# Performance work log

Hardware: AMD Instinct MI355X
Metric: run time of the kernel (lower is better)

## Reference

```python
import jax, jax.numpy as jnp
import numpy as np

B, S, H, E = 4, 4096, 4096, 64
TOP_K = 2


def setup_inputs() -> dict:
    key = jax.random.key(0)
    k1, k2 = jax.random.split(key)
    x = jax.random.normal(k1, (B, S, H), dtype=jnp.float32)
    # nn.Linear weight: [num_experts, hidden_size]
    gate_w = jax.random.normal(k2, (E, H), dtype=jnp.float32) * (1.0 / np.sqrt(H))
    return {"x": x, "gate_w": gate_w}


def reference(x, gate_w):
    # gate linear: [B,S,H] @ [H,E] -> [B,S,E]
    router_logits = jnp.einsum("bsh,eh->bse", x, gate_w)
    router_weights = jax.nn.softmax(router_logits, axis=-1)
    topk_weights, topk_indices = jax.lax.top_k(router_weights, TOP_K)  # [B,S,2]
    topk_weights = topk_weights / jnp.sum(topk_weights, axis=-1, keepdims=True)
    return topk_weights, topk_indices
```

## Files before the change

kernel.cpp:

```cpp
#include <hip/hip_runtime.h>
#include <math.h>


typedef _Float16 half8 __attribute__((ext_vector_type(8)));
typedef float floatx4 __attribute__((ext_vector_type(4)));

constexpr int Hdim = 4096;
constexpr int Edim = 64;
constexpr int NTOK = 16384;
constexpr int BK   = 128;
constexpr int NKT  = Hdim / BK;
constexpr float SCL  = 2048.0f;
constexpr float ISCL = 1.0f / 2048.0f;

__device__ alignas(16) _Float16 g_whf[(size_t)Edim * Hdim];
__device__ alignas(16) _Float16 g_wlf[(size_t)Edim * Hdim];

#define GLD_LDS16(gp, lp)                                              \
    __builtin_amdgcn_global_load_lds(                                  \
        (const __attribute__((address_space(1))) void*)(gp),           \
        (__attribute__((address_space(3))) void*)(lp), 16, 0, 0)

__global__ __launch_bounds__(256)
void wconv_kernel(const float* __restrict__ gw)
{
    const int n    = blockIdx.x * 256 + threadIdx.x;
    const int lane = n & 63;
    const int frag = n >> 6;
    const int nt   = frag & 3;
    const int kc   = frag >> 2;
    const int e    = nt * 16 + (lane & 15);
    const int k0   = kc * 32 + (lane >> 4) * 8;

    const float* src = gw + (size_t)e * Hdim + k0;
    const float4 v0 = *(const float4*)src;
    const float4 v1 = *(const float4*)(src + 4);
    const float* p0 = (const float*)&v0;
    const float* p1 = (const float*)&v1;
    half8 h, l;
    #pragma unroll
    for (int c = 0; c < 4; ++c) {
        _Float16 hh = (_Float16)p0[c];
        h[c] = hh;
        l[c] = (_Float16)((p0[c] - (float)hh) * SCL);
        hh = (_Float16)p1[c];
        h[c + 4] = hh;
        l[c + 4] = (_Float16)((p1[c] - (float)hh) * SCL);
    }
    *(half8*)(g_whf + (size_t)n * 8) = h;
    *(half8*)(g_wlf + (size_t)n * 8) = l;
}

__global__ __launch_bounds__(256, 4)
void router_kernel(const float* __restrict__ x,
                   float* __restrict__ out)
{
    __shared__ alignas(16) float  sx[3][16 * BK];
    __shared__ alignas(16) float4 sc[4][16];

    const int tid  = threadIdx.x;
    const int w    = tid >> 6;
    const int lane = tid & 63;
    const int ln15 = lane & 15;
    const int quad = lane >> 4;
    const int sw   = ln15 & 7;
    const int t0   = blockIdx.x * 16;

    const int r0 = w * 4 + (lane >> 5);
    const int r1 = r0 + 2;
    const int g0 = (lane & 31) ^ (r0 & 7);
    const int g1 = (lane & 31) ^ (r1 & 7);
    const float* px0 = x + (size_t)(t0 + r0) * Hdim + g0 * 4;
    const float* px1 = x + (size_t)(t0 + r1) * Hdim + g1 * 4;

    const _Float16* whw = g_whf + (size_t)w * 512 + lane * 8;
    const _Float16* wlw = g_wlf + (size_t)w * 512 + lane * 8;

    floatx4 accm = (floatx4)0.0f, accc = (floatx4)0.0f, accl = (floatx4)0.0f;

    auto cvt8 = [&](const float4& a, const float4& b, half8& h, half8& l) {
        const float* pa = (const float*)&a;
        const float* pb = (const float*)&b;
        #pragma unroll
        for (int c = 0; c < 4; ++c) {
            _Float16 hh = (_Float16)pa[c];
            h[c] = hh;
            l[c] = (_Float16)((pa[c] - (float)hh) * SCL);
            hh = (_Float16)pb[c];
            h[c + 4] = hh;
            l[c + 4] = (_Float16)((pb[c] - (float)hh) * SCL);
        }
    };

    half8 bhA[4], blA[4], bhB[4], blB[4];

    #pragma unroll
    for (int c = 0; c < 4; ++c) {
        bhA[c] = *(const half8*)(whw + (size_t)c * 2048);
        blA[c] = *(const half8*)(wlw + (size_t)c * 2048);
    }
    GLD_LDS16(px0,      &sx[0][w * 512]);
    GLD_LDS16(px1,      &sx[0][w * 512 + 256]);
    GLD_LDS16(px0 + BK, &sx[1][w * 512]);
    GLD_LDS16(px1 + BK, &sx[1][w * 512 + 256]);

    auto step = [&](int kt, half8 (&bch)[4], half8 (&bcl)[4],
                            half8 (&bnh)[4], half8 (&bnl)[4]) {
        const int ktn = (kt + 1) & (NKT - 1);
        #pragma unroll
        for (int c = 0; c < 4; ++c) {
            bnh[c] = *(const half8*)(whw + (size_t)(ktn * 4 + c) * 2048);
            bnl[c] = *(const half8*)(wlw + (size_t)(ktn * 4 + c) * 2048);
        }
        __builtin_amdgcn_sched_barrier(0);

        const int ts = (kt + 2) & (NKT - 1);
        const int tb = (kt + 2) % 3;
        GLD_LDS16(px0 + (size_t)ts * BK, &sx[tb][w * 512]);
        GLD_LDS16(px1 + (size_t)ts * BK, &sx[tb][w * 512 + 256]);

        asm volatile("s_waitcnt vmcnt(12)" ::: "memory");
        asm volatile("s_barrier" ::: "memory");

        const int cur = kt % 3;
        #pragma unroll
        for (int c = 0; c < 4; ++c) {
            const int s0 = (c * 8 + quad * 2) ^ sw;
            const float4 f0 = *(const float4*)&sx[cur][ln15 * BK + s0 * 4];
            const float4 f1 = *(const float4*)&sx[cur][ln15 * BK + (s0 ^ 1) * 4];
            half8 ah, al;
            cvt8(f0, f1, ah, al);
            accm = __builtin_amdgcn_mfma_f32_16x16x32_f16(ah, bch[c], accm, 0, 0, 0);
            accc = __builtin_amdgcn_mfma_f32_16x16x32_f16(ah, bcl[c], accc, 0, 0, 0);
            accc = __builtin_amdgcn_mfma_f32_16x16x32_f16(al, bch[c], accc, 0, 0, 0);
            accl = __builtin_amdgcn_mfma_f32_16x16x32_f16(al, bcl[c], accl, 0, 0, 0);
        }
        asm volatile("s_barrier" ::: "memory");
    };

    for (int kt = 0; kt < NKT; kt += 2) {
        step(kt,     bhA, blA, bhB, blB);
        step(kt + 1, bhB, blB, bhA, blA);
    }
    __syncthreads();

    const floatx4 vv = accm + accc * ISCL + accl * (ISCL * ISCL);

    #pragma unroll
    for (int i = 0; i < 4; ++i) {
        float m1 = vv[i], m2 = -INFINITY;
        int i1 = w * 16 + ln15, i2 = 0;
        #pragma unroll
        for (int mk = 1; mk <= 8; mk <<= 1) {
            const float om1 = __shfl_xor(m1, mk);
            const int   oi1 = __shfl_xor(i1, mk);
            const float om2 = __shfl_xor(m2, mk);
            const int   oi2 = __shfl_xor(i2, mk);
            const bool aw = (m1 > om1) || (m1 == om1 && i1 < oi1);
            const float w1v = aw ? m1 : om1;  const int w1i = aw ? i1 : oi1;
            const float ca  = aw ? m2 : om2;  const int cai = aw ? i2 : oi2;
            const float cb  = aw ? om1 : m1;  const int cbi = aw ? oi1 : i1;
            const bool sw2 = (ca > cb) || (ca == cb && cai < cbi);
            m1 = w1v; i1 = w1i;
            m2 = sw2 ? ca : cb;
            i2 = sw2 ? cai : cbi;
        }
        if (ln15 == 0)
            sc[w][quad * 4 + i] = float4{m1, m2, (float)i1, (float)i2};
    }
    __syncthreads();

    if (tid < 16) {
        float4 c = sc[0][tid];
        float m1 = c.x, m2 = c.y, i1 = c.z, i2 = c.w;
        #pragma unroll
        for (int q = 1; q < 4; ++q) {
            c = sc[q][tid];
            const float om1 = c.x, om2 = c.y, oi1 = c.z, oi2 = c.w;
            const bool aw = (m1 > om1) || (m1 == om1 && i1 < oi1);
            const float w1v = aw ? m1 : om1;  const float w1i = aw ? i1 : oi1;
            const float ca  = aw ? m2 : om2;  const float cai = aw ? i2 : oi2;
            const float cb  = aw ? om1 : m1;  const float cbi = aw ? oi1 : i1;
            const bool sw2 = (ca > cb) || (ca == cb && cai < cbi);
            m1 = w1v; i1 = w1i;
            m2 = sw2 ? ca : cb;
            i2 = sw2 ? cai : cbi;
        }
        const float r   = expf(m2 - m1);
        const float inv = 1.0f / (1.0f + r);
        const int t = t0 + tid;
        float* ow = out + 2 * (size_t)t;
        ow[0] = inv;
        ow[1] = r * inv;
        float* oi = out + 2 * (size_t)NTOK + 2 * (size_t)t;
        oi[0] = i1;
        oi[1] = i2;
    }
}

extern "C" void kernel_launch(void* const* d_in, const int* in_sizes, int n_in,
                              void* d_out, int out_size, void* d_ws, size_t ws_size,
                              hipStream_t stream) {
    const float* x  = (const float*)d_in[0];
    const float* gw = (const float*)d_in[1];
    float* out = (float*)d_out;
    (void)d_ws; (void)ws_size;

    hipLaunchKernelGGL(wconv_kernel, dim3(128), dim3(256), 0, stream, gw);
    hipLaunchKernelGGL(router_kernel, dim3(NTOK / 16), dim3(256), 0, stream,
                       x, out);
}
```

Measured before the change: 376.2 us.

## Convert x tile to fp16 hi/lo once in LDS and double token tile

Before, each of the four waves converted the same 16 token rows from fp32 to the fp16 hi/lo split for its own 16 experts, so the conversion ran four times. Now each tile is converted once cooperatively into shared fp16 buffers, and the block covers 32 tokens with two M-tiles per wave. This halves the weight-fragment loads per token and removes the redundant conversion work. In exchange it adds LDS traffic, an extra conversion stage in the pipeline, more registers and LDS per block, and occupancy drops from 4 to 3 blocks.

```diff
diff --git a/kernel.cpp b/kernel.cpp
--- a/kernel.cpp
+++ b/kernel.cpp
@@ -8,7 +8,8 @@
 constexpr int Hdim = 4096;
 constexpr int Edim = 64;
 constexpr int NTOK = 16384;
-constexpr int BK   = 128;
+constexpr int BM   = 32;
+constexpr int BK   = 64;
 constexpr int NKT  = Hdim / BK;
 constexpr float SCL  = 2048.0f;
 constexpr float ISCL = 1.0f / 2048.0f;
@@ -51,32 +52,46 @@
     *(half8*)(g_wlf + (size_t)n * 8) = l;
 }
 
-__global__ __launch_bounds__(256, 4)
+__global__ __launch_bounds__(256, 3)
 void router_kernel(const float* __restrict__ x,
                    float* __restrict__ out)
 {
-    __shared__ alignas(16) float  sx[3][16 * BK];
-    __shared__ alignas(16) float4 sc[4][16];
+    __shared__ alignas(16) float    sraw[3][BM * BK];
+    __shared__ alignas(16) _Float16 sxh[2][BM * BK];
+    __shared__ alignas(16) _Float16 sxl[2][BM * BK];
+    __shared__ alignas(16) float4   sc[4][BM];
 
     const int tid  = threadIdx.x;
     const int w    = tid >> 6;
     const int lane = tid & 63;
     const int ln15 = lane & 15;
     const int quad = lane >> 4;
-    const int sw   = ln15 & 7;
-    const int t0   = blockIdx.x * 16;
-
-    const int r0 = w * 4 + (lane >> 5);
-    const int r1 = r0 + 2;
-    const int g0 = (lane & 31) ^ (r0 & 7);
-    const int g1 = (lane & 31) ^ (r1 & 7);
-    const float* px0 = x + (size_t)(t0 + r0) * Hdim + g0 * 4;
-    const float* px1 = x + (size_t)(t0 + r1) * Hdim + g1 * 4;
+    const int t0   = blockIdx.x * BM;
+
+    const int r0  = 8 * w + (lane >> 4);
+    const int r1  = r0 + 4;
+    const int gg0 = (lane & 15) ^ (r0 & 7);
+    const int gg1 = (lane & 15) ^ (r1 & 7);
+    const float* px0 = x + (size_t)(t0 + r0) * Hdim + gg0 * 4;
+    const float* px1 = x + (size_t)(t0 + r1) * Hdim + gg1 * 4;
+
+    const int cr  = 8 * w + ((tid >> 3) & 7);
+    const int cc  = tid & 7;
+    const int crs = cr & 7;
+    const int rdA = cr * BK + (((2 * cc)     ^ crs) << 2);
+    const int rdB = cr * BK + (((2 * cc + 1) ^ crs) << 2);
+    const int wrS = cr * BK + ((cc ^ crs) << 3);
 
     const _Float16* whw = g_whf + (size_t)w * 512 + lane * 8;
     const _Float16* wlw = g_wlf + (size_t)w * 512 + lane * 8;
 
-    floatx4 accm = (floatx4)0.0f, accc = (floatx4)0.0f, accl = (floatx4)0.0f;
+    floatx4 accm[2], accc[2], accl[2];
+    #pragma unroll
+    for (int mt = 0; mt < 2; ++mt) {
+        accm[mt] = (floatx4)0.0f;
+        accc[mt] = (floatx4)0.0f;
+        accl[mt] = (floatx4)0.0f;
+    }
 
     auto cvt8 = [&](const float4& a, const float4& b, half8& h, half8& l) {
         const float* pa = (const float*)&a;
@@ -92,50 +107,67 @@
         }
     };
 
-    half8 bhA[4], blA[4], bhB[4], blB[4];
-
-    #pragma unroll
-    for (int c = 0; c < 4; ++c) {
+    auto convert = [&](int rb, int sb) {
+        const float4 f0 = *(const float4*)&sraw[rb][rdA];
+        const float4 f1 = *(const float4*)&sraw[rb][rdB];
+        half8 h, l;
+        cvt8(f0, f1, h, l);
+        *(half8*)&sxh[sb][wrS] = h;
+        *(half8*)&sxl[sb][wrS] = l;
+    };
+
+    half8 bhA[2], blA[2], bhB[2], blB[2];
+
+    GLD_LDS16(px0 + 0 * BK, &sraw[0][(8 * w) * BK]);
+    GLD_LDS16(px1 + 0 * BK, &sraw[0][(8 * w + 4) * BK]);
+    GLD_LDS16(px0 + 1 * BK, &sraw[1][(8 * w) * BK]);
+    GLD_LDS16(px1 + 1 * BK, &sraw[1][(8 * w + 4) * BK]);
+    #pragma unroll
+    for (int c = 0; c < 2; ++c) {
         bhA[c] = *(const half8*)(whw + (size_t)c * 2048);
         blA[c] = *(const half8*)(wlw + (size_t)c * 2048);
     }
-    GLD_LDS16(px0,      &sx[0][w * 512]);
-    GLD_LDS16(px1,      &sx[0][w * 512 + 256]);
-    GLD_LDS16(px0 + BK, &sx[1][w * 512]);
-    GLD_LDS16(px1 + BK, &sx[1][w * 512 + 256]);
-
-    auto step = [&](int kt, half8 (&bch)[4], half8 (&bcl)[4],
-                            half8 (&bnh)[4], half8 (&bnl)[4]) {
+    GLD_LDS16(px0 + 2 * BK, &sraw[2][(8 * w) * BK]);
+    GLD_LDS16(px1 + 2 * BK, &sraw[2][(8 * w + 4) * BK]);
+
+    asm volatile("s_waitcnt vmcnt(8)" ::: "memory");
+    convert(0, 0);
+
+    auto step = [&](int kt, half8 (&bch)[2], half8 (&bcl)[2],
+                            half8 (&bnh)[2], half8 (&bnl)[2]) {
         const int ktn = (kt + 1) & (NKT - 1);
         #pragma unroll
-        for (int c = 0; c < 4; ++c) {
-            bnh[c] = *(const half8*)(whw + (size_t)(ktn * 4 + c) * 2048);
-            bnl[c] = *(const half8*)(wlw + (size_t)(ktn * 4 + c) * 2048);
-        }
+        for (int c = 0; c < 2; ++c) {
+            bnh[c] = *(const half8*)(whw + (size_t)(2 * ktn + c) * 2048);
+            bnl[c] = *(const half8*)(wlw + (size_t)(2 * ktn + c) * 2048);
+        }
+        const int ts = (kt + 3) & (NKT - 1);
+        const int tb = (kt + 3) % 3;
+        GLD_LDS16(px0 + (size_t)ts * BK, &sraw[tb][(8 * w) * BK]);
+        GLD_LDS16(px1 + (size_t)ts * BK, &sraw[tb][(8 * w + 4) * BK]);
+
+        asm volatile("s_waitcnt vmcnt(8)" ::: "memory");
+        asm volatile("s_waitcnt lgkmcnt(0)" ::: "memory");
         __builtin_amdgcn_sched_barrier(0);
-
-        const int ts = (kt + 2) & (NKT - 1);
-        const int tb = (kt + 2) % 3;
-        GLD_LDS16(px0 + (size_t)ts * BK, &sx[tb][w * 512]);
-        GLD_LDS16(px1 + (size_t)ts * BK, &sx[tb][w * 512 + 256]);
-
-        asm volatile("s_waitcnt vmcnt(12)" ::: "memory");
         asm volatile("s_barrier" ::: "memory");
 
-        const int cur = kt % 3;
-        #pragma unroll
-        for (int c = 0; c < 4; ++c) {
-            const int s0 = (c * 8 + quad * 2) ^ sw;
-            const float4 f0 = *(const float4*)&sx[cur][ln15 * BK + s0 * 4];
-            const float4 f1 = *(const float4*)&sx[cur][ln15 * BK + (s0 ^ 1) * 4];
-            half8 ah, al;
-            cvt8(f0, f1, ah, al);
-            accm = __builtin_amdgcn_mfma_f32_16x16x32_f16(ah, bch[c], accm, 0, 0, 0);
-            accc = __builtin_amdgcn_mfma_f32_16x16x32_f16(ah, bcl[c], accc, 0, 0, 0);
-            accc = __builtin_amdgcn_mfma_f32_16x16x32_f16(al, bch[c], accc, 0, 0, 0);
-            accl = __builtin_amdgcn_mfma_f32_16x16x32_f16(al, bcl[c], accl, 0, 0, 0);
-        }
-        asm volatile("s_barrier" ::: "memory");
+        convert((kt + 1) % 3, (kt + 1) & 1);
+
+        const int cb = kt & 1;
+        #pragma unroll
+        for (int c = 0; c < 2; ++c) {
+            #pragma unroll
+            for (int mt = 0; mt < 2; ++mt) {
+                const int row = mt * 16 + ln15;
+                const int sA  = row * BK + (((c * 4 + quad) ^ (row & 7)) << 3);
+                const half8 ah = *(const half8*)&sxh[cb][sA];
+                const half8 al = *(const half8*)&sxl[cb][sA];
+                accm[mt] = __builtin_amdgcn_mfma_f32_16x16x32_f16(ah, bch[c], accm[mt], 0, 0, 0);
+                accc[mt] = __builtin_amdgcn_mfma_f32_16x16x32_f16(ah, bcl[c], accc[mt], 0, 0, 0);
+                accc[mt] = __builtin_amdgcn_mfma_f32_16x16x32_f16(al, bch[c], accc[mt], 0, 0, 0);
+                accl[mt] = __builtin_amdgcn_mfma_f32_16x16x32_f16(al, bcl[c], accl[mt], 0, 0, 0);
+            }
+        }
     };
 
     for (int kt = 0; kt < NKT; kt += 2) {
@@ -144,33 +176,35 @@
     }
     __syncthreads();
 
-    const floatx4 vv = accm + accc * ISCL + accl * (ISCL * ISCL);
-
-    #pragma unroll
-    for (int i = 0; i < 4; ++i) {
-        float m1 = vv[i], m2 = -INFINITY;
-        int i1 = w * 16 + ln15, i2 = 0;
-        #pragma unroll
-        for (int mk = 1; mk <= 8; mk <<= 1) {
-            const float om1 = __shfl_xor(m1, mk);
-            const int   oi1 = __shfl_xor(i1, mk);
-            const float om2 = __shfl_xor(m2, mk);
-            const int   oi2 = __shfl_xor(i2, mk);
-            const bool aw = (m1 > om1) || (m1 == om1 && i1 < oi1);
-            const float w1v = aw ? m1 : om1;  const int w1i = aw ? i1 : oi1;
-            const float ca  = aw ? m2 : om2;  const int cai = aw ? i2 : oi2;
-            const float cb  = aw ? om1 : m1;  const int cbi = aw ? oi1 : i1;
-            const bool sw2 = (ca > cb) || (ca == cb && cai < cbi);
-            m1 = w1v; i1 = w1i;
-            m2 = sw2 ? ca : cb;
-            i2 = sw2 ? cai : cbi;
-        }
-        if (ln15 == 0)
-            sc[w][quad * 4 + i] = float4{m1, m2, (float)i1, (float)i2};
+    #pragma unroll
+    for (int mt = 0; mt < 2; ++mt) {
+        const floatx4 vv = accm[mt] + accc[mt] * ISCL + accl[mt] * (ISCL * ISCL);
+        #pragma unroll
+        for (int i = 0; i < 4; ++i) {
+            float m1 = vv[i], m2 = -INFINITY;
+            int i1 = w * 16 + ln15, i2 = 0;
+            #pragma unroll
+            for (int mk = 1; mk <= 8; mk <<= 1) {
+                const float om1 = __shfl_xor(m1, mk);
+                const int   oi1 = __shfl_xor(i1, mk);
+                const float om2 = __shfl_xor(m2, mk);
+                const int   oi2 = __shfl_xor(i2, mk);
+                const bool aw = (m1 > om1) || (m1 == om1 && i1 < oi1);
+                const float w1v = aw ? m1 : om1;  const int w1i = aw ? i1 : oi1;
+                const float ca  = aw ? m2 : om2;  const int cai = aw ? i2 : oi2;
+                const float cb  = aw ? om1 : m1;  const int cbi = aw ? oi1 : i1;
+                const bool sw2 = (ca > cb) || (ca == cb && cai < cbi);
+                m1 = w1v; i1 = w1i;
+                m2 = sw2 ? ca : cb;
+                i2 = sw2 ? cai : cbi;
+            }
+            if (ln15 == 0)
+                sc[w][mt * 16 + quad * 4 + i] = float4{m1, m2, (float)i1, (float)i2};
+        }
     }
     __syncthreads();
 
-    if (tid < 16) {
+    if (tid < BM) {
         float4 c = sc[0][tid];
         float m1 = c.x, m2 = c.y, i1 = c.z, i2 = c.w;
         #pragma unroll
@@ -207,6 +241,6 @@
     (void)d_ws; (void)ws_size;
 
     hipLaunchKernelGGL(wconv_kernel, dim3(128), dim3(256), 0, stream, gw);
-    hipLaunchKernelGGL(router_kernel, dim3(NTOK / 16), dim3(256), 0, stream,
+    hipLaunchKernelGGL(router_kernel, dim3(NTOK / BM), dim3(256), 0, stream,
                        x, out);
 }
```

After: 387.1 us. 1.03x slower.
